# Kernel optimization log

Hardware: AMD Instinct MI355X
Metric: run time of the kernel (lower is better)

The kernel has to match this reference:

```python
import jax, jax.numpy as jnp
import numpy as np

N, C, H, W = 32, 49, 9, 9   # batch, spectral bands (=outplane), spatial patch
MSIZE, K, PAD = 24, 7, 3    # conv3d out channels, spectral kernel, padding
EPS = 1e-5


def setup_inputs() -> dict:
    key = jax.random.key(0)
    k1, k2, k3 = jax.random.split(key, 3)
    x = jax.random.normal(k1, (N, C, H, W), dtype=jnp.float32)
    # Conv3d(1, MSIZE, [7,1,1]) params, PyTorch default uniform init
    fan_in = 1 * K * 1 * 1
    bound = 1.0 / np.sqrt(fan_in)
    conv_w = jax.random.uniform(k2, (MSIZE, 1, K, 1, 1), jnp.float32, -bound, bound)
    conv_b = jax.random.uniform(k3, (MSIZE,), jnp.float32, -bound, bound)
    # BatchNorm2d(49) affine params at init
    gamma = jnp.ones((C,), jnp.float32)
    beta = jnp.zeros((C,), jnp.float32)
    return {"x": x, "conv_w": conv_w, "conv_b": conv_b, "gamma": gamma, "beta": beta}


def reference(x, conv_w, conv_b, gamma, beta):
    n, c, h, w = x.shape
    # Conv3d over (depth=spectral, h, w) with kernel [K,1,1]: depth preserved
    x5 = x[:, None]  # (n,1,c,h,w)
    m = jax.lax.conv_general_dilated(
        x5, conv_w, window_strides=(1, 1, 1),
        padding=[(PAD, PAD), (0, 0), (0, 0)],
        dimension_numbers=("NCDHW", "OIDHW", "NCDHW"),
    ) + conv_b[None, :, None, None, None]        # (n, MSIZE, c, h, w)
    d = m.shape[1] * m.shape[2]                   # d = MSIZE * c
    mask = jax.nn.softmax(m.reshape(n, d, h * w), axis=-1).reshape(n, d, h, w)
    # original computes convm0 twice -> mask1 == mask0; reuse `mask` for both
    fk = jnp.einsum("ndhw,nchw->ncd", mask, x)    # (n, c, d)
    # out[n,c,h,w] = sum_d leaky_relu(fk[n,c,d] * mask[n,d,h,w])
    big = jnp.einsum("ncd,ndhw->ncdhw", fk, mask)  # (n,c,d,h,w) large intermediate
    out = jax.nn.leaky_relu(big, negative_slope=0.01).sum(axis=2)
    out = out + x                                  # residual
    # BatchNorm2d in training mode: batch statistics over (n,h,w) per channel
    mean = out.mean(axis=(0, 2, 3))
    var = out.var(axis=(0, 2, 3))
    out = (out - mean[:, None, None]) * jax.lax.rsqrt(var[:, None, None] + EPS)
    out = out * gamma[:, None, None] + beta[:, None, None]
    return out
```

## Files before the change

### kernel.cpp

```cpp
#include <hip/hip_runtime.h>
#include <hip/hip_bf16.h>

#define NN    32
#define CC    49
#define HWSZ  81
#define MSZ   24
#define KSZ   7
#define PADSZ 3
#define NHW   (NN*HWSZ)
#define NCHW  (NN*CC*HWSZ)

#define XSB_S  104
#define MSK_S  104
#define MSKT_S 72
#define G_S    72

typedef __attribute__((ext_vector_type(8))) short short8;
typedef __attribute__((ext_vector_type(4))) short short4v;
typedef __attribute__((ext_vector_type(4))) float f32x4;

__device__ __forceinline__ short f2b(float v) {
    unsigned u = __float_as_uint(v);
    u += 0x7fffu + ((u >> 16) & 1u);
    return (short)(u >> 16);
}
__device__ __forceinline__ float b2f(short s) {
    return __uint_as_float(((unsigned)(unsigned short)s) << 16);
}

__global__ __launch_bounds__(256) void fuse_k1(
    const float* __restrict__ x, const float* __restrict__ cw,
    const float* __restrict__ cb, float* __restrict__ acc,
    float* __restrict__ stats, int use_ws)
{
    __shared__ short xsb [64 * XSB_S];
    __shared__ short msk [64 * MSK_S];
    __shared__ short mskT[96 * MSKT_S];
    __shared__ short gm  [64 * G_S];

    const int o = blockIdx.x;
    const int n = blockIdx.y;
    const int t = threadIdx.x;
    const int lane = t & 63;
    const int wv = t >> 6;
    const int lr = lane & 15;
    const int lq = lane >> 4;

    if (use_ws && o == 0 && n == 0 && t < 98) stats[t] = 0.f;

    {
        f32x4 z = {0.f, 0.f, 0.f, 0.f};
        for (int i = t; i < 832; i += 256) {
            ((f32x4*)xsb)[i] = z;
            ((f32x4*)msk)[i] = z;
        }
        for (int i = t; i < 864; i += 256)
            ((f32x4*)mskT)[i] = z;
    }

    const float* xg = x + (size_t)n * CC * HWSZ;
    float wk[KSZ];
    #pragma unroll
    for (int k = 0; k < KSZ; ++k) wk[k] = cw[o * KSZ + k];
    const float bias = cb[o];
    __syncthreads();

    for (int i = t; i < CC * HWSZ; i += 256) {
        int c = i / HWSZ, hw = i - c * HWSZ;
        xsb[c * XSB_S + hw] = f2b(xg[i]);
    }
    __syncthreads();

    #pragma unroll
    for (int it = 0; it < 4; ++it) {
        int dd = it * 16 + wv * 4 + lq;
        if (dd < CC) {
            float a0 = 0.f, a1 = 0.f, a2 = 0.f, a3 = 0.f, a4 = 0.f, a5 = 0.f;
            #pragma unroll
            for (int k = 0; k < KSZ; ++k) {
                int r = dd + k - PADSZ;
                if (r >= 0 && r < CC) {
                    const short* xr = xsb + r * XSB_S;
                    float w = wk[k];
                    a0 += w * b2f(xr[lr]);
                    a1 += w * b2f(xr[lr + 16]);
                    a2 += w * b2f(xr[lr + 32]);
                    a3 += w * b2f(xr[lr + 48]);
                    a4 += w * b2f(xr[lr + 64]);
                    if (lr == 0) a5 += w * b2f(xr[80]);
                }
            }
            a0 += bias; a1 += bias; a2 += bias; a3 += bias; a4 += bias;
            a5 = (lr == 0) ? (a5 + bias) : -1e30f;
            float mx = fmaxf(fmaxf(fmaxf(a0, a1), fmaxf(a2, a3)), fmaxf(a4, a5));
            #pragma unroll
            for (int off = 8; off; off >>= 1) mx = fmaxf(mx, __shfl_xor(mx, off, 64));
            float e0 = __expf(a0 - mx), e1 = __expf(a1 - mx), e2 = __expf(a2 - mx);
            float e3 = __expf(a3 - mx), e4 = __expf(a4 - mx);
            float e5 = (lr == 0) ? __expf(a5 - mx) : 0.f;
            float s = e0 + e1 + e2 + e3 + e4 + e5;
            #pragma unroll
            for (int off = 8; off; off >>= 1) s += __shfl_xor(s, off, 64);
            float inv = 1.f / s;
            short b0 = f2b(e0 * inv), b1 = f2b(e1 * inv), b2 = f2b(e2 * inv);
            short b3 = f2b(e3 * inv), b4 = f2b(e4 * inv);
            short* mrow = msk + dd * MSK_S;
            mrow[lr]      = b0;  mskT[(lr     ) * MSKT_S + dd] = b0;
            mrow[lr + 16] = b1;  mskT[(lr + 16) * MSKT_S + dd] = b1;
            mrow[lr + 32] = b2;  mskT[(lr + 32) * MSKT_S + dd] = b2;
            mrow[lr + 48] = b3;  mskT[(lr + 48) * MSKT_S + dd] = b3;
            mrow[lr + 64] = b4;  mskT[(lr + 64) * MSKT_S + dd] = b4;
            if (lr == 0) {
                short b5 = f2b(e5 * inv);
                mrow[80] = b5;   mskT[80 * MSKT_S + dd] = b5;
            }
        }
    }
    __syncthreads();

    {
        short8 a2[3];
        #pragma unroll
        for (int ks = 0; ks < 3; ++ks)
            a2[ks] = *(const short8*)&msk[(wv * 16 + lr) * MSK_S + ks * 32 + lq * 8];
        #pragma unroll
        for (int nt = 0; nt < 4; ++nt) {
            f32x4 accv = {0.f, 0.f, 0.f, 0.f};
            #pragma unroll
            for (int ks = 0; ks < 3; ++ks) {
                short8 b = *(const short8*)&xsb[(nt * 16 + lr) * XSB_S + ks * 32 + lq * 8];
                accv = __builtin_amdgcn_mfma_f32_16x16x32_bf16(a2[ks], b, accv, 0, 0, 0);
            }
            short4v pk;
            #pragma unroll
            for (int r = 0; r < 4; ++r) {
                float v = accv[r];
                v = (v >= 0.f) ? v : 0.01f * v;
                pk[r] = f2b(v);
            }
            *(short4v*)&gm[(nt * 16 + lr) * G_S + wv * 16 + lq * 4] = pk;
        }
    }
    __syncthreads();

    {
        float* dstn = use_ws ? (acc + (size_t)(o * NN + n) * CC * HWSZ)
                             : (acc + (size_t)n * CC * HWSZ);
        short8 a1[2];
        #pragma unroll
        for (int ks = 0; ks < 2; ++ks)
            a1[ks] = *(const short8*)&gm[(wv * 16 + lr) * G_S + ks * 32 + lq * 8];
        #pragma unroll
        for (int nt = 0; nt < 6; ++nt) {
            f32x4 accv = {0.f, 0.f, 0.f, 0.f};
            #pragma unroll
            for (int ks = 0; ks < 2; ++ks) {
                short8 b = *(const short8*)&mskT[(nt * 16 + lr) * MSKT_S + ks * 32 + lq * 8];
                accv = __builtin_amdgcn_mfma_f32_16x16x32_bf16(a1[ks], b, accv, 0, 0, 0);
            }
            int hw = nt * 16 + lr;
            if (hw < HWSZ) {
                int cb = wv * 16 + lq * 4;
                if (use_ws) {
                    #pragma unroll
                    for (int r = 0; r < 4; ++r) {
                        int c = cb + r;
                        if (c < CC) dstn[c * HWSZ + hw] = accv[r];
                    }
                } else {
                    #pragma unroll
                    for (int r = 0; r < 4; ++r) {
                        int c = cb + r;
                        if (c < CC) atomicAdd(dstn + c * HWSZ + hw, accv[r]);
                    }
                }
            }
        }
    }
}

__global__ __launch_bounds__(256) void fuse_k2a(
    const float* __restrict__ ws, const float* __restrict__ x,
    float* __restrict__ out, float* __restrict__ stats)
{
    const int c = blockIdx.x;
    const int s = blockIdx.y;
    const int t = threadIdx.x;
    float sum = 0.f, sq = 0.f;
    for (int i = t; i < 8 * HWSZ; i += 256) {
        int n = 8 * s + i / HWSZ;
        int hw = i - (i / HWSZ) * HWSZ;
        int idx = (n * CC + c) * HWSZ + hw;
        float v = x[idx];
        #pragma unroll
        for (int o = 0; o < MSZ; ++o) v += ws[(size_t)o * NCHW + idx];
        out[idx] = v;
        sum += v; sq += v * v;
    }
    #pragma unroll
    for (int off = 32; off; off >>= 1) {
        sum += __shfl_xor(sum, off, 64);
        sq  += __shfl_xor(sq, off, 64);
    }
    __shared__ float rs[4], rq[4];
    const int lane = t & 63, wv = t >> 6;
    if (lane == 0) { rs[wv] = sum; rq[wv] = sq; }
    __syncthreads();
    if (t == 0) {
        float ts = rs[0] + rs[1] + rs[2] + rs[3];
        float tq = rq[0] + rq[1] + rq[2] + rq[3];
        atomicAdd(&stats[c], ts);
        atomicAdd(&stats[CC + c], tq);
    }
}

__global__ __launch_bounds__(256) void fuse_k2b(
    float* __restrict__ out, const float* __restrict__ stats,
    const float* __restrict__ gamma, const float* __restrict__ beta)
{
    int i = blockIdx.x * 256 + threadIdx.x;
    if (i < NCHW) {
        int c = (i / HWSZ) % CC;
        const float invD = 1.f / (float)NHW;
        float mean = stats[c] * invD;
        float var  = stats[CC + c] * invD - mean * mean;
        float scal = rsqrtf(var + 1e-5f) * gamma[c];
        out[i] = (out[i] - mean) * scal + beta[c];
    }
}

__global__ __launch_bounds__(1024) void fuse_k2(
    float* __restrict__ out, const float* __restrict__ x,
    const float* __restrict__ gamma, const float* __restrict__ beta)
{
    const int c = blockIdx.x;
    const int t = threadIdx.x;
    float vals[3];
    float sum = 0.f, sq = 0.f;
    int cnt = 0;
    for (int i = t; i < NHW; i += 1024) {
        int n = i / HWSZ;
        int hw = i - n * HWSZ;
        int idx = (n * CC + c) * HWSZ + hw;
        float v = out[idx] + x[idx];
        vals[cnt++] = v;
        sum += v; sq += v * v;
    }
    #pragma unroll
    for (int off = 32; off; off >>= 1) {
        sum += __shfl_xor(sum, off, 64);
        sq  += __shfl_xor(sq, off, 64);
    }
    __shared__ float rs[16], rq[16];
    const int lane = t & 63, wv = t >> 6;
    if (lane == 0) { rs[wv] = sum; rq[wv] = sq; }
    __syncthreads();
    float ts = 0.f, tq = 0.f;
    #pragma unroll
    for (int w = 0; w < 16; ++w) { ts += rs[w]; tq += rq[w]; }
    const float invD = 1.f / (float)NHW;
    float mean = ts * invD;
    float var  = tq * invD - mean * mean;
    float scal = rsqrtf(var + 1e-5f) * gamma[c];
    float shft = beta[c] - mean * scal;
    cnt = 0;
    for (int i = t; i < NHW; i += 1024) {
        int n = i / HWSZ;
        int hw = i - n * HWSZ;
        out[(n * CC + c) * HWSZ + hw] = vals[cnt++] * scal + shft;
    }
}

extern "C" void kernel_launch(void* const* d_in, const int* in_sizes, int n_in,
                              void* d_out, int out_size, void* d_ws, size_t ws_size,
                              hipStream_t stream) {
    const float* x     = (const float*)d_in[0];
    const float* cw    = (const float*)d_in[1];
    const float* cb    = (const float*)d_in[2];
    const float* gamma = (const float*)d_in[3];
    const float* beta  = (const float*)d_in[4];
    float* out = (float*)d_out;

    const size_t need = (size_t)MSZ * NCHW * sizeof(float) + 2 * CC * sizeof(float);
    if (ws_size >= need) {
        float* ws    = (float*)d_ws;
        float* stats = ws + (size_t)MSZ * NCHW;
        fuse_k1<<<dim3(MSZ, NN), 256, 0, stream>>>(x, cw, cb, ws, stats, 1);
        fuse_k2a<<<dim3(CC, 4), 256, 0, stream>>>(ws, x, out, stats);
        fuse_k2b<<<(NCHW + 255) / 256, 256, 0, stream>>>(out, stats, gamma, beta);
    } else {
        hipMemsetAsync(out, 0, (size_t)NCHW * sizeof(float), stream);
        fuse_k1<<<dim3(MSZ, NN), 256, 0, stream>>>(x, cw, cb, out, nullptr, 0);
        fuse_k2<<<CC, 1024, 0, stream>>>(out, x, gamma, beta);
    }
}
```

Measured before the change: 85.51 us.

## Fuse batchnorm stats and normalize via grid barrier; vectorize LDS accesses

Merges the reduction and normalization kernels into one launch. The 196 blocks sum their channel statistics, then spin on a global arrival counter (a software grid barrier) before applying the normalization to values they kept in registers. This removes one kernel launch and a full re-read and re-write of the output. In fuse_k1, the shared-memory zeroing now clears only the padding regions, and the conv reads and mask writes use 4-wide short vectors. The spin barrier depends on all 196 blocks being resident at once, which holds on this GPU, but the counter is never reset between calls except through the stats zeroing in k1.

```diff
diff --git a/kernel.cpp b/kernel.cpp
--- a/kernel.cpp
+++ b/kernel.cpp
@@ -46,29 +46,32 @@
     const int lr = lane & 15;
     const int lq = lane >> 4;
 
-    if (use_ws && o == 0 && n == 0 && t < 98) stats[t] = 0.f;
-
-    {
-        f32x4 z = {0.f, 0.f, 0.f, 0.f};
-        for (int i = t; i < 832; i += 256) {
-            ((f32x4*)xsb)[i] = z;
-            ((f32x4*)msk)[i] = z;
-        }
-        for (int i = t; i < 864; i += 256)
-            ((f32x4*)mskT)[i] = z;
-    }
+    if (use_ws && o == 0 && n == 0 && t < 99) stats[t] = 0.f;
 
     const float* xg = x + (size_t)n * CC * HWSZ;
     float wk[KSZ];
     #pragma unroll
     for (int k = 0; k < KSZ; ++k) wk[k] = cw[o * KSZ + k];
     const float bias = cb[o];
-    __syncthreads();
-
+
+    const f32x4 z4 = {0.f, 0.f, 0.f, 0.f};
     for (int i = t; i < CC * HWSZ; i += 256) {
         int c = i / HWSZ, hw = i - c * HWSZ;
         xsb[c * XSB_S + hw] = f2b(xg[i]);
     }
+    if (t < CC) {
+        short* row = xsb + t * XSB_S;
+        #pragma unroll
+        for (int cq = 81; cq < 88; ++cq) row[cq] = 0;
+        *(f32x4*)(row + 88) = z4;
+        *(f32x4*)(row + 96) = z4;
+    }
+    for (int j = t; j < 15 * 13; j += 256) {
+        int rr = j / 13, cg = j - rr * 13;
+        *(f32x4*)(xsb + (49 + rr) * XSB_S + cg * 8) = z4;
+    }
+    for (int i = t; i < 832; i += 256) ((f32x4*)msk)[i] = z4;
+    for (int i = t; i < 864; i += 256) ((f32x4*)mskT)[i] = z4;
     __syncthreads();
 
     #pragma unroll
@@ -81,12 +84,13 @@
                 int r = dd + k - PADSZ;
                 if (r >= 0 && r < CC) {
                     const short* xr = xsb + r * XSB_S;
+                    short4v xa = *(const short4v*)(xr + 4 * lr);
                     float w = wk[k];
-                    a0 += w * b2f(xr[lr]);
-                    a1 += w * b2f(xr[lr + 16]);
-                    a2 += w * b2f(xr[lr + 32]);
-                    a3 += w * b2f(xr[lr + 48]);
-                    a4 += w * b2f(xr[lr + 64]);
+                    a0 += w * b2f(xa[0]);
+                    a1 += w * b2f(xa[1]);
+                    a2 += w * b2f(xa[2]);
+                    a3 += w * b2f(xa[3]);
+                    a4 += w * b2f(xr[64 + lr]);
                     if (lr == 0) a5 += w * b2f(xr[80]);
                 }
             }
@@ -102,17 +106,22 @@
             #pragma unroll
             for (int off = 8; off; off >>= 1) s += __shfl_xor(s, off, 64);
             float inv = 1.f / s;
-            short b0 = f2b(e0 * inv), b1 = f2b(e1 * inv), b2 = f2b(e2 * inv);
-            short b3 = f2b(e3 * inv), b4 = f2b(e4 * inv);
+            short4v pk;
+            pk[0] = f2b(e0 * inv); pk[1] = f2b(e1 * inv);
+            pk[2] = f2b(e2 * inv); pk[3] = f2b(e3 * inv);
+            short b4 = f2b(e4 * inv);
             short* mrow = msk + dd * MSK_S;
-            mrow[lr]      = b0;  mskT[(lr     ) * MSKT_S + dd] = b0;
-            mrow[lr + 16] = b1;  mskT[(lr + 16) * MSKT_S + dd] = b1;
-            mrow[lr + 32] = b2;  mskT[(lr + 32) * MSKT_S + dd] = b2;
-            mrow[lr + 48] = b3;  mskT[(lr + 48) * MSKT_S + dd] = b3;
-            mrow[lr + 64] = b4;  mskT[(lr + 64) * MSKT_S + dd] = b4;
+            *(short4v*)(mrow + 4 * lr) = pk;
+            mrow[64 + lr] = b4;
+            mskT[(4 * lr    ) * MSKT_S + dd] = pk[0];
+            mskT[(4 * lr + 1) * MSKT_S + dd] = pk[1];
+            mskT[(4 * lr + 2) * MSKT_S + dd] = pk[2];
+            mskT[(4 * lr + 3) * MSKT_S + dd] = pk[3];
+            mskT[(64 + lr   ) * MSKT_S + dd] = b4;
             if (lr == 0) {
                 short b5 = f2b(e5 * inv);
-                mrow[80] = b5;   mskT[80 * MSKT_S + dd] = b5;
+                mrow[80] = b5;
+                mskT[80 * MSKT_S + dd] = b5;
             }
         }
     }
@@ -179,22 +188,26 @@
     }
 }
 
-__global__ __launch_bounds__(256) void fuse_k2a(
+__global__ __launch_bounds__(256) void fuse_k2f(
     const float* __restrict__ ws, const float* __restrict__ x,
-    float* __restrict__ out, float* __restrict__ stats)
+    float* __restrict__ out, float* __restrict__ stats,
+    const float* __restrict__ gamma, const float* __restrict__ beta)
 {
     const int c = blockIdx.x;
     const int s = blockIdx.y;
     const int t = threadIdx.x;
+    float vals[3];
+    int   idxs[3];
+    int cnt = 0;
     float sum = 0.f, sq = 0.f;
     for (int i = t; i < 8 * HWSZ; i += 256) {
-        int n = 8 * s + i / HWSZ;
+        int nn = 8 * s + i / HWSZ;
         int hw = i - (i / HWSZ) * HWSZ;
-        int idx = (n * CC + c) * HWSZ + hw;
+        int idx = (nn * CC + c) * HWSZ + hw;
         float v = x[idx];
         #pragma unroll
         for (int o = 0; o < MSZ; ++o) v += ws[(size_t)o * NCHW + idx];
-        out[idx] = v;
+        vals[cnt] = v; idxs[cnt] = idx; ++cnt;
         sum += v; sq += v * v;
     }
     #pragma unroll
@@ -202,7 +215,7 @@
         sum += __shfl_xor(sum, off, 64);
         sq  += __shfl_xor(sq, off, 64);
     }
-    __shared__ float rs[4], rq[4];
+    __shared__ float rs[4], rq[4], bshare[2];
     const int lane = t & 63, wv = t >> 6;
     if (lane == 0) { rs[wv] = sum; rq[wv] = sq; }
     __syncthreads();
@@ -211,22 +224,23 @@
         float tq = rq[0] + rq[1] + rq[2] + rq[3];
         atomicAdd(&stats[c], ts);
         atomicAdd(&stats[CC + c], tq);
-    }
-}
-
-__global__ __launch_bounds__(256) void fuse_k2b(
-    float* __restrict__ out, const float* __restrict__ stats,
-    const float* __restrict__ gamma, const float* __restrict__ beta)
-{
-    int i = blockIdx.x * 256 + threadIdx.x;
-    if (i < NCHW) {
-        int c = (i / HWSZ) % CC;
-        const float invD = 1.f / (float)NHW;
-        float mean = stats[c] * invD;
-        float var  = stats[CC + c] * invD - mean * mean;
-        float scal = rsqrtf(var + 1e-5f) * gamma[c];
-        out[i] = (out[i] - mean) * scal + beta[c];
-    }
+        __threadfence();
+        unsigned* cntp = (unsigned*)(stats + 2 * CC);
+        atomicAdd(cntp, 1u);
+        while (atomicAdd(cntp, 0u) < (unsigned)(CC * 4))
+            __builtin_amdgcn_s_sleep(8);
+        __threadfence();
+        bshare[0] = atomicAdd(&stats[c], 0.f);
+        bshare[1] = atomicAdd(&stats[CC + c], 0.f);
+    }
+    __syncthreads();
+    const float invD = 1.f / (float)NHW;
+    float mean = bshare[0] * invD;
+    float var  = bshare[1] * invD - mean * mean;
+    float scal = rsqrtf(var + 1e-5f) * gamma[c];
+    float shft = beta[c] - mean * scal;
+    for (int j = 0; j < cnt; ++j)
+        out[idxs[j]] = vals[j] * scal + shft;
 }
 
 __global__ __launch_bounds__(1024) void fuse_k2(
@@ -281,13 +295,12 @@
     const float* beta  = (const float*)d_in[4];
     float* out = (float*)d_out;
 
-    const size_t need = (size_t)MSZ * NCHW * sizeof(float) + 2 * CC * sizeof(float);
+    const size_t need = (size_t)MSZ * NCHW * sizeof(float) + 128 * sizeof(float);
     if (ws_size >= need) {
         float* ws    = (float*)d_ws;
         float* stats = ws + (size_t)MSZ * NCHW;
         fuse_k1<<<dim3(MSZ, NN), 256, 0, stream>>>(x, cw, cb, ws, stats, 1);
-        fuse_k2a<<<dim3(CC, 4), 256, 0, stream>>>(ws, x, out, stats);
-        fuse_k2b<<<(NCHW + 255) / 256, 256, 0, stream>>>(out, stats, gamma, beta);
+        fuse_k2f<<<dim3(CC, 4), 256, 0, stream>>>(ws, x, out, stats, gamma, beta);
     } else {
         hipMemsetAsync(out, 0, (size_t)NCHW * sizeof(float), stream);
         fuse_k1<<<dim3(MSZ, NN), 256, 0, stream>>>(x, cw, cb, out, nullptr, 0);
```

New measurement: 93.20 us. +9.0%, slower.
